# Performance work log

Measured on AMD Instinct MI355X. Metric: run time of the kernel, lower is better.

The kernel has to match this reference:

```python
import jax, jax.numpy as jnp
import numpy as np


def setup_inputs() -> dict:
    key = jax.random.key(0)
    ks = jax.random.split(key, 6)
    B, S, D = 2, 2048, 1024
    E, DFF = 8, 2048  # E includes always-on expert 0; router sees E-1 routed experts
    scale = 0.02
    return {
        "hidden_states": jax.random.normal(ks[0], (B, S, D), dtype=jnp.float32),
        "router_w": jax.random.normal(ks[1], (D, E - 1), dtype=jnp.float32) * scale,
        "router_b": jnp.zeros((E - 1,), dtype=jnp.float32),
        "wg": jax.random.normal(ks[2], (E, D, DFF), dtype=jnp.float32) * scale,
        "wu": jax.random.normal(ks[3], (E, D, DFF), dtype=jnp.float32) * scale,
        "wd": jax.random.normal(ks[4], (E, DFF, D), dtype=jnp.float32) * scale,
        "top_k": 2,
    }


def _expert_mlp(x, wg_e, wu_e, wd_e):
    # SwiGLU MLP: down( silu(x @ gate) * (x @ up) )
    return (jax.nn.silu(x @ wg_e) * (x @ wu_e)) @ wd_e


def reference(hidden_states, router_w, router_b, wg, wu, wd, top_k):
    B, S, D = hidden_states.shape
    E = wg.shape[0]  # total experts incl. always-on expert 0
    x = hidden_states.reshape(-1, D)  # [T, D]
    T = x.shape[0]

    # Router over E-1 routed experts, softmax in float32
    router_logits = x @ router_w + router_b  # [T, E-1]
    probs = jax.nn.softmax(router_logits.astype(jnp.float32), axis=-1)
    topw, topi = jax.lax.top_k(probs, top_k)  # [T, k]
    topw = topw / jnp.sum(topw, axis=-1, keepdims=True)
    topw = topw.astype(x.dtype)

    # Dense combine weights over routed experts (0 for unselected)
    cw = jnp.zeros((T, E - 1), dtype=x.dtype)
    cw = cw.at[jnp.arange(T)[:, None], topi].add(topw)  # [T, E-1]

    # Always-on expert 0 with weight 1
    out = _expert_mlp(x, wg[0], wu[0], wd[0])  # [T, D]

    # Routed experts 1..E-1 (static small loop over experts)
    for e in range(1, E):
        ye = _expert_mlp(x, wg[e], wu[e], wd[e])  # [T, D]
        out = out + cw[:, e - 1, None] * ye

    return out.reshape(B, S, -1)
```

## Files before the change

kernel.cpp:

```cpp
#include <hip/hip_runtime.h>

#define T_TOK 4096
#define DIM   1024
#define DFF   2048
#define NE    8
#define NR    7
#define MAXNB 71
#define NY    (32 + MAXNB)

typedef __bf16 bf16x8 __attribute__((ext_vector_type(8)));
typedef float  floatx4 __attribute__((ext_vector_type(4)));

__device__ __forceinline__ unsigned short f32_bf16(float f) {
  union { float f; unsigned int u; } v; v.f = f;
  unsigned int u = v.u;
  unsigned int r = (u + 0x7FFFu + ((u >> 16) & 1u)) >> 16;
  return (unsigned short)r;
}

typedef __attribute__((address_space(3))) void lds_void_t;
typedef const __attribute__((address_space(1))) void g_void_t;

__device__ __forceinline__ void gld16(const void* g, void* l) {
  __builtin_amdgcn_global_load_lds((g_void_t*)g, (lds_void_t*)l, 16, 0, 0);
}

__global__ __launch_bounds__(256) void cvt_x_kernel(const float4* __restrict__ in,
                                                    ushort4* __restrict__ out) {
  int i = blockIdx.x * 256 + threadIdx.x;
  float4 v = in[i];
  ushort4 o;
  o.x = f32_bf16(v.x); o.y = f32_bf16(v.y);
  o.z = f32_bf16(v.z); o.w = f32_bf16(v.w);
  out[i] = o;
}

__global__ __launch_bounds__(256) void router_kernel(const float* __restrict__ x,
                                                     const float* __restrict__ rw,
                                                     const float* __restrict__ rb,
                                                     int* __restrict__ idxAll,
                                                     float* __restrict__ wslAll,
                                                     int* __restrict__ cnt) {
  const int lane = threadIdx.x & 63;
  const int t = blockIdx.x * 4 + (threadIdx.x >> 6);
  const float* xr = x + (size_t)t * DIM;
  float acc[NR];
#pragma unroll
  for (int e = 0; e < NR; e++) acc[e] = 0.f;
  for (int d = lane; d < DIM; d += 64) {
    float xv = xr[d];
#pragma unroll
    for (int e = 0; e < NR; e++) acc[e] += xv * rw[d * NR + e];
  }
#pragma unroll
  for (int off = 32; off > 0; off >>= 1) {
#pragma unroll
    for (int e = 0; e < NR; e++) acc[e] += __shfl_xor(acc[e], off, 64);
  }
  if (lane == 0) {
    idxAll[t] = t; wslAll[t] = 1.0f;
    float lg[NR];
    float m = -1e30f;
#pragma unroll
    for (int e = 0; e < NR; e++) { lg[e] = acc[e] + rb[e]; m = fmaxf(m, lg[e]); }
    float p[NR], s = 0.f;
#pragma unroll
    for (int e = 0; e < NR; e++) { p[e] = expf(lg[e] - m); s += p[e]; }
#pragma unroll
    for (int e = 0; e < NR; e++) p[e] /= s;
    int i1 = 0;
#pragma unroll
    for (int e = 1; e < NR; e++) if (p[e] > p[i1]) i1 = e;
    int i2 = (i1 == 0) ? 1 : 0;
#pragma unroll
    for (int e = 0; e < NR; e++) if (e != i1 && p[e] > p[i2]) i2 = e;
    float w1 = p[i1], w2 = p[i2], sw = w1 + w2;
    int s1 = atomicAdd(&cnt[i1], 1);
    idxAll[4096 + i1 * 4096 + s1] = t; wslAll[4096 + i1 * 4096 + s1] = w1 / sw;
    int s2 = atomicAdd(&cnt[i2], 1);
    idxAll[4096 + i2 * 4096 + s2] = t; wslAll[4096 + i2 * 4096 + s2] = w2 / sw;
  }
}

__global__ __launch_bounds__(256) void sched_kernel(const int* __restrict__ cnt,
                                                    int* __restrict__ idxAll,
                                                    float* __restrict__ wslAll,
                                                    int4* __restrict__ schedAll,
                                                    int4* __restrict__ schedP,
                                                    int rsb) {
  __shared__ int nb[NR], pref[NR];
  if (threadIdx.x == 0) {
    int p = 0;
    for (int e = 0; e < NR; e++) { int c = cnt[e]; int n = (c + 127) >> 7; nb[e] = n; pref[e] = p; p += n; }
  }
  __syncthreads();
  for (int e = 0; e < NR; e++) {
    int c = cnt[e], top = nb[e] * 128;
    for (int i = c + (int)threadIdx.x; i < top; i += 256) {
      idxAll[4096 + e * 4096 + i] = 0; wslAll[4096 + e * 4096 + i] = 0.f;
    }
  }
  const int NBtot = pref[NR - 1] + nb[NR - 1];
  for (int y = threadIdx.x; y < 32; y += 256) {
    int4 ent; ent.x = 0; ent.y = y * 128; ent.z = y * 128; ent.w = 0;
    schedAll[y] = ent;
  }
  for (int y = threadIdx.x; y < MAXNB; y += 256) {
    int4 ent; ent.x = -1; ent.y = 0; ent.z = 0; ent.w = 0;
    if (y < NBtot) {
#pragma unroll
      for (int e = 0; e < NR; e++)
        if (y >= pref[e] && y < pref[e] + nb[e]) {
          int rb2 = y - pref[e];
          ent.x = e + 1; ent.y = 4096 + e * 4096 + rb2 * 128; ent.z = rsb + y * 128;
        }
    }
    schedAll[32 + y] = ent;
  }
  for (int i = threadIdx.x; i < NR * 32; i += 256) {
    int e = i >> 5, rb2 = i & 31;
    int4 ent; ent.w = 0;
    if (rb2 < nb[e]) { ent.x = e + 1; ent.y = 4096 + e * 4096 + rb2 * 128; ent.z = rsb + rb2 * 128; }
    else             { ent.x = -1; ent.y = 0; ent.z = 0; }
    schedP[i] = ent;
  }
}

__global__ __launch_bounds__(256) void transpose_cvt_kernel(
    const float* __restrict__ wg, const float* __restrict__ wu, const float* __restrict__ wd,
    unsigned short* __restrict__ wgt, unsigned short* __restrict__ wut,
    unsigned short* __restrict__ wdt) {
  __shared__ float tile[64][33];
  const int z = blockIdx.z;
  const float* src; unsigned short* dst; int R, C;
  if (z < 8)       { src = wg + (size_t)z * DIM * DFF;        dst = wgt + (size_t)z * DIM * DFF;        R = DIM; C = DFF; }
  else if (z < 16) { src = wu + (size_t)(z - 8) * DIM * DFF;  dst = wut + (size_t)(z - 8) * DIM * DFF;  R = DIM; C = DFF; }
  else             { src = wd + (size_t)(z - 16) * DFF * DIM; dst = wdt + (size_t)(z - 16) * DFF * DIM; R = DFF; C = DIM; }
  const int c0 = blockIdx.x * 32, r0 = blockIdx.y * 64;
  if (c0 >= C || r0 >= R) return;
  const int tx = threadIdx.x & 31, ty = threadIdx.x >> 5;
#pragma unroll
  for (int j = ty; j < 64; j += 8)
    tile[j][tx] = src[(size_t)(r0 + j) * C + c0 + tx];
  __syncthreads();
#pragma unroll
  for (int j = ty; j < 32; j += 8) {
    unsigned int lo = f32_bf16(tile[2 * tx][j]);
    unsigned int hi = f32_bf16(tile[2 * tx + 1][j]);
    *(unsigned int*)(dst + (size_t)(c0 + j) * R + r0 + 2 * tx) = lo | (hi << 16);
  }
}

__global__ __launch_bounds__(256) void gemm1_kernel(
    const unsigned short* __restrict__ xb, const unsigned short* __restrict__ wgt,
    const unsigned short* __restrict__ wut, const int* __restrict__ idxAll,
    const int4* __restrict__ sched, unsigned short* __restrict__ h) {
  const int4 ent = sched[blockIdx.y];
  if (ent.x < 0) return;
  __shared__ unsigned short As[128 * 32];
  __shared__ unsigned short Bg[64 * 32];
  __shared__ unsigned short Bu[64 * 32];
  const int tid = threadIdx.x, lane = tid & 63, wid = tid >> 6;
  const int n0 = blockIdx.x * 64;
  const int wm = (wid >> 1) * 64, wn = (wid & 1) * 32;
  floatx4 accg[4][2], accu[4][2];
  const floatx4 z4 = {0.f, 0.f, 0.f, 0.f};
#pragma unroll
  for (int i = 0; i < 4; i++)
#pragma unroll
    for (int j = 0; j < 2; j++) { accg[i][j] = z4; accu[i][j] = z4; }
  const unsigned short* wgt_e = wgt + (size_t)ent.x * DIM * DFF;
  const unsigned short* wut_e = wut + (size_t)ent.x * DIM * DFF;
  const int srow = tid >> 2, scol = (tid & 3) * 8;
  const int tok0 = idxAll[ent.y + srow];
  const int tok1 = idxAll[ent.y + srow + 64];
  const unsigned short* ap0 = xb + (size_t)tok0 * DIM + scol;
  const unsigned short* ap1 = xb + (size_t)tok1 * DIM + scol;
  const unsigned short* bgp = wgt_e + (size_t)(n0 + srow) * DIM + scol;
  const unsigned short* bup = wut_e + (size_t)(n0 + srow) * DIM + scol;
  unsigned short* as0 = As + tid * 8;
  unsigned short* as1 = As + (256 + tid) * 8;
  unsigned short* bgl = Bg + tid * 8;
  unsigned short* bul = Bu + tid * 8;
  const int fr = lane & 15, kq = (lane >> 4) * 8;
  for (int k0 = 0; k0 < DIM; k0 += 32) {
    __syncthreads();
    gld16(ap0 + k0, as0); gld16(ap1 + k0, as1);
    gld16(bgp + k0, bgl); gld16(bup + k0, bul);
    __syncthreads();
    bf16x8 af[4], bgf[2], buf2[2];
#pragma unroll
    for (int mi = 0; mi < 4; mi++) af[mi] = *(const bf16x8*)(As + (wm + mi * 16 + fr) * 32 + kq);
#pragma unroll
    for (int ni = 0; ni < 2; ni++) {
      bgf[ni]  = *(const bf16x8*)(Bg + (wn + ni * 16 + fr) * 32 + kq);
      buf2[ni] = *(const bf16x8*)(Bu + (wn + ni * 16 + fr) * 32 + kq);
    }
#pragma unroll
    for (int mi = 0; mi < 4; mi++)
#pragma unroll
      for (int ni = 0; ni < 2; ni++) {
        accg[mi][ni] = __builtin_amdgcn_mfma_f32_16x16x32_bf16(af[mi], bgf[ni], accg[mi][ni], 0, 0, 0);
        accu[mi][ni] = __builtin_amdgcn_mfma_f32_16x16x32_bf16(af[mi], buf2[ni], accu[mi][ni], 0, 0, 0);
      }
  }
  const int rb0 = wm + (lane >> 4) * 4;
  const int cb0 = n0 + wn + fr;
#pragma unroll
  for (int mi = 0; mi < 4; mi++)
#pragma unroll
    for (int ni = 0; ni < 2; ni++)
#pragma unroll
      for (int r = 0; r < 4; r++) {
        int lrow = rb0 + mi * 16 + r;
        int col = cb0 + ni * 16;
        float g = accg[mi][ni][r], u = accu[mi][ni][r];
        float hv = (g / (1.f + __expf(-g))) * u;
        h[(size_t)(ent.z + lrow) * DFF + col] = f32_bf16(hv);
      }
}

__global__ __launch_bounds__(256) void gemm2_kernel(
    const unsigned short* __restrict__ h, const unsigned short* __restrict__ wdt,
    const int* __restrict__ idxAll, const float* __restrict__ wslAll,
    const int4* __restrict__ sched, float* __restrict__ out) {
  const int4 ent = sched[blockIdx.y];
  if (ent.x < 0) return;
  __shared__ unsigned short As[128 * 32];
  __shared__ unsigned short Bs[128 * 32];
  const int tid = threadIdx.x, lane = tid & 63, wid = tid >> 6;
  const int n0 = blockIdx.x * 128;
  const int wm = (wid >> 1) * 64, wn = (wid & 1) * 64;
  floatx4 acc[4][4];
  const floatx4 z4 = {0.f, 0.f, 0.f, 0.f};
#pragma unroll
  for (int i = 0; i < 4; i++)
#pragma unroll
    for (int j = 0; j < 4; j++) acc[i][j] = z4;
  const unsigned short* wdt_e = wdt + (size_t)ent.x * DFF * DIM;
  const int srow = tid >> 2, scol = (tid & 3) * 8;
  const unsigned short* ap0 = h + (size_t)(ent.z + srow) * DFF + scol;
  const unsigned short* ap1 = ap0 + (size_t)64 * DFF;
  const unsigned short* bp0 = wdt_e + (size_t)(n0 + srow) * DFF + scol;
  const unsigned short* bp1 = bp0 + (size_t)64 * DFF;
  unsigned short* as0 = As + tid * 8;
  unsigned short* as1 = As + (256 + tid) * 8;
  unsigned short* bs0 = Bs + tid * 8;
  unsigned short* bs1 = Bs + (256 + tid) * 8;
  const int fr = lane & 15, kq = (lane >> 4) * 8;
  for (int k0 = 0; k0 < DFF; k0 += 32) {
    __syncthreads();
    gld16(ap0 + k0, as0); gld16(ap1 + k0, as1);
    gld16(bp0 + k0, bs0); gld16(bp1 + k0, bs1);
    __syncthreads();
    bf16x8 af[4], bf[4];
#pragma unroll
    for (int mi = 0; mi < 4; mi++) af[mi] = *(const bf16x8*)(As + (wm + mi * 16 + fr) * 32 + kq);
#pragma unroll
    for (int ni = 0; ni < 4; ni++) bf[ni] = *(const bf16x8*)(Bs + (wn + ni * 16 + fr) * 32 + kq);
#pragma unroll
    for (int mi = 0; mi < 4; mi++)
#pragma unroll
      for (int ni = 0; ni < 4; ni++)
        acc[mi][ni] = __builtin_amdgcn_mfma_f32_16x16x32_bf16(af[mi], bf[ni], acc[mi][ni], 0, 0, 0);
  }
  const int rb0 = wm + (lane >> 4) * 4;
  const int cb0 = n0 + wn + fr;
#pragma unroll
  for (int mi = 0; mi < 4; mi++)
#pragma unroll
    for (int r = 0; r < 4; r++) {
      int lrow = rb0 + mi * 16 + r;
      int tok = idxAll[ent.y + lrow];
      float s = wslAll[ent.y + lrow];
      if (s != 0.f) {
#pragma unroll
        for (int ni = 0; ni < 4; ni++)
          atomicAdd(&out[(size_t)tok * DIM + cb0 + ni * 16], s * acc[mi][ni][r]);
      }
    }
}

extern "C" void kernel_launch(void* const* d_in, const int* in_sizes, int n_in,
                              void* d_out, int out_size, void* d_ws, size_t ws_size,
                              hipStream_t stream) {
  const float* x  = (const float*)d_in[0];
  const float* rw = (const float*)d_in[1];
  const float* rb = (const float*)d_in[2];
  const float* wg = (const float*)d_in[3];
  const float* wu = (const float*)d_in[4];
  const float* wd = (const float*)d_in[5];
  float* out = (float*)d_out;

  const bool modeA = ws_size >= (size_t)163321408;
  const bool modeB = !modeA && ws_size >= (size_t)146544192;
  const size_t H_ROWS = modeA ? 13184 : (modeB ? 9088 : 4096);
  const int rsb = modeA ? 4096 : 0;

  char* p = (char*)d_ws;
  unsigned short* xb  = (unsigned short*)p; p += (size_t)T_TOK * DIM * 2;
  unsigned short* h   = (unsigned short*)p; p += H_ROWS * DFF * 2;
  unsigned short* wgt = (unsigned short*)p; p += (size_t)NE * DIM * DFF * 2;
  unsigned short* wut = (unsigned short*)p; p += (size_t)NE * DIM * DFF * 2;
  unsigned short* wdt = (unsigned short*)p; p += (size_t)NE * DIM * DFF * 2;
  int*   idxAll = (int*)p;   p += (size_t)(4096 + NR * 4096) * 4;
  float* wslAll = (float*)p; p += (size_t)(4096 + NR * 4096) * 4;
  int*   cnt = (int*)p;      p += 64;
  int4*  schedAll = (int4*)p; p += 2048;
  int4*  schedP   = (int4*)p; p += 4096;

  cvt_x_kernel<<<dim3(T_TOK * DIM / 4 / 256), 256, 0, stream>>>((const float4*)x, (ushort4*)xb);
  hipMemsetAsync(cnt, 0, 64, stream);
  hipMemsetAsync(out, 0, (size_t)out_size * 4, stream);
  router_kernel<<<dim3(T_TOK / 4), 256, 0, stream>>>(x, rw, rb, idxAll, wslAll, cnt);
  sched_kernel<<<dim3(1), 256, 0, stream>>>(cnt, idxAll, wslAll, schedAll, schedP, rsb);
  transpose_cvt_kernel<<<dim3(64, 32, 24), 256, 0, stream>>>(wg, wu, wd, wgt, wut, wdt);

  if (modeA) {
    gemm1_kernel<<<dim3(DFF / 64, NY), 256, 0, stream>>>(xb, wgt, wut, idxAll, schedAll, h);
    gemm2_kernel<<<dim3(DIM / 128, NY), 256, 0, stream>>>(h, wdt, idxAll, wslAll, schedAll, out);
  } else if (modeB) {
    gemm1_kernel<<<dim3(DFF / 64, 32), 256, 0, stream>>>(xb, wgt, wut, idxAll, schedAll, h);
    gemm2_kernel<<<dim3(DIM / 128, 32), 256, 0, stream>>>(h, wdt, idxAll, wslAll, schedAll, out);
    gemm1_kernel<<<dim3(DFF / 64, MAXNB), 256, 0, stream>>>(xb, wgt, wut, idxAll, schedAll + 32, h);
    gemm2_kernel<<<dim3(DIM / 128, MAXNB), 256, 0, stream>>>(h, wdt, idxAll, wslAll, schedAll + 32, out);
  } else {
    gemm1_kernel<<<dim3(DFF / 64, 32), 256, 0, stream>>>(xb, wgt, wut, idxAll, schedAll, h);
    gemm2_kernel<<<dim3(DIM / 128, 32), 256, 0, stream>>>(h, wdt, idxAll, wslAll, schedAll, out);
    for (int e = 0; e < NR; e++) {
      gemm1_kernel<<<dim3(DFF / 64, 32), 256, 0, stream>>>(xb, wgt, wut, idxAll, schedP + e * 32, h);
      gemm2_kernel<<<dim3(DIM / 128, 32), 256, 0, stream>>>(h, wdt, idxAll, wslAll, schedP + e * 32, out);
    }
  }
}
```

Baseline: 627.2 us.

## Replace atomic scatter-add with dense expert outputs plus combine kernel; widen gemm1 tile

In the large-workspace mode, gemm2 now writes per-row expert outputs densely into a scratch buffer that aliases the gate-weight copy once gemm1 is done. A new combine kernel then gathers each token's shared-expert row and its two routed rows and applies the routing weights, which removes the float atomics and the output memset. gemm1 moves to a 128-column tile with launch bounds set for 2 blocks per CU, doubling the reuse of A loads. The shared expert's token indices are now computed directly instead of read from an index array. This adds an extra pass over a large fp32 buffer and more register pressure in gemm1, and it relies on careful buffer aliasing (routing weights placed in wdt, y in wgt).

```diff
diff --git a/kernel.cpp b/kernel.cpp
--- a/kernel.cpp
+++ b/kernel.cpp
@@ -38,9 +38,11 @@
 __global__ __launch_bounds__(256) void router_kernel(const float* __restrict__ x,
                                                      const float* __restrict__ rw,
                                                      const float* __restrict__ rb,
-                                                     int* __restrict__ idxAll,
-                                                     float* __restrict__ wslAll,
-                                                     int* __restrict__ cnt) {
+                                                     int* __restrict__ idxR,
+                                                     float* __restrict__ wslR,
+                                                     int* __restrict__ cnt,
+                                                     int4* __restrict__ tokE,
+                                                     float2* __restrict__ tokW) {
   const int lane = threadIdx.x & 63;
   const int t = blockIdx.x * 4 + (threadIdx.x >> 6);
   const float* xr = x + (size_t)t * DIM;
@@ -58,7 +60,6 @@
     for (int e = 0; e < NR; e++) acc[e] += __shfl_xor(acc[e], off, 64);
   }
   if (lane == 0) {
-    idxAll[t] = t; wslAll[t] = 1.0f;
     float lg[NR];
     float m = -1e30f;
 #pragma unroll
@@ -75,18 +76,24 @@
 #pragma unroll
     for (int e = 0; e < NR; e++) if (e != i1 && p[e] > p[i2]) i2 = e;
     float w1 = p[i1], w2 = p[i2], sw = w1 + w2;
+    float w1n = w1 / sw, w2n = w2 / sw;
     int s1 = atomicAdd(&cnt[i1], 1);
-    idxAll[4096 + i1 * 4096 + s1] = t; wslAll[4096 + i1 * 4096 + s1] = w1 / sw;
+    idxR[i1 * 4096 + s1] = t; wslR[i1 * 4096 + s1] = w1n;
     int s2 = atomicAdd(&cnt[i2], 1);
-    idxAll[4096 + i2 * 4096 + s2] = t; wslAll[4096 + i2 * 4096 + s2] = w2 / sw;
+    idxR[i2 * 4096 + s2] = t; wslR[i2 * 4096 + s2] = w2n;
+    int4 te; te.x = i1; te.y = s1; te.z = i2; te.w = s2;
+    tokE[t] = te;
+    float2 tw; tw.x = w1n; tw.y = w2n;
+    tokW[t] = tw;
   }
 }
 
 __global__ __launch_bounds__(256) void sched_kernel(const int* __restrict__ cnt,
-                                                    int* __restrict__ idxAll,
-                                                    float* __restrict__ wslAll,
+                                                    int* __restrict__ idxR,
+                                                    float* __restrict__ wslR,
                                                     int4* __restrict__ schedAll,
                                                     int4* __restrict__ schedP,
+                                                    int* __restrict__ prefOut,
                                                     int rsb) {
   __shared__ int nb[NR], pref[NR];
   if (threadIdx.x == 0) {
@@ -94,15 +101,16 @@
     for (int e = 0; e < NR; e++) { int c = cnt[e]; int n = (c + 127) >> 7; nb[e] = n; pref[e] = p; p += n; }
   }
   __syncthreads();
+  if (threadIdx.x < NR) prefOut[threadIdx.x] = pref[threadIdx.x];
   for (int e = 0; e < NR; e++) {
     int c = cnt[e], top = nb[e] * 128;
     for (int i = c + (int)threadIdx.x; i < top; i += 256) {
-      idxAll[4096 + e * 4096 + i] = 0; wslAll[4096 + e * 4096 + i] = 0.f;
+      idxR[e * 4096 + i] = 0; wslR[e * 4096 + i] = 0.f;
     }
   }
   const int NBtot = pref[NR - 1] + nb[NR - 1];
   for (int y = threadIdx.x; y < 32; y += 256) {
-    int4 ent; ent.x = 0; ent.y = y * 128; ent.z = y * 128; ent.w = 0;
+    int4 ent; ent.x = 0; ent.y = -1; ent.z = y * 128; ent.w = 0;
     schedAll[y] = ent;
   }
   for (int y = threadIdx.x; y < MAXNB; y += 256) {
@@ -112,7 +120,7 @@
       for (int e = 0; e < NR; e++)
         if (y >= pref[e] && y < pref[e] + nb[e]) {
           int rb2 = y - pref[e];
-          ent.x = e + 1; ent.y = 4096 + e * 4096 + rb2 * 128; ent.z = rsb + y * 128;
+          ent.x = e + 1; ent.y = e * 4096 + rb2 * 128; ent.z = rsb + y * 128;
         }
     }
     schedAll[32 + y] = ent;
@@ -120,7 +128,7 @@
   for (int i = threadIdx.x; i < NR * 32; i += 256) {
     int e = i >> 5, rb2 = i & 31;
     int4 ent; ent.w = 0;
-    if (rb2 < nb[e]) { ent.x = e + 1; ent.y = 4096 + e * 4096 + rb2 * 128; ent.z = rsb + rb2 * 128; }
+    if (rb2 < nb[e]) { ent.x = e + 1; ent.y = e * 4096 + rb2 * 128; ent.z = rb2 * 128; }
     else             { ent.x = -1; ent.y = 0; ent.z = 0; }
     schedP[i] = ent;
   }
@@ -151,55 +159,61 @@
   }
 }
 
-__global__ __launch_bounds__(256) void gemm1_kernel(
+__global__ __launch_bounds__(256, 2) void gemm1_kernel(
     const unsigned short* __restrict__ xb, const unsigned short* __restrict__ wgt,
-    const unsigned short* __restrict__ wut, const int* __restrict__ idxAll,
+    const unsigned short* __restrict__ wut, const int* __restrict__ idxR,
     const int4* __restrict__ sched, unsigned short* __restrict__ h) {
   const int4 ent = sched[blockIdx.y];
   if (ent.x < 0) return;
   __shared__ unsigned short As[128 * 32];
-  __shared__ unsigned short Bg[64 * 32];
-  __shared__ unsigned short Bu[64 * 32];
+  __shared__ unsigned short Bg[128 * 32];
+  __shared__ unsigned short Bu[128 * 32];
   const int tid = threadIdx.x, lane = tid & 63, wid = tid >> 6;
-  const int n0 = blockIdx.x * 64;
-  const int wm = (wid >> 1) * 64, wn = (wid & 1) * 32;
-  floatx4 accg[4][2], accu[4][2];
+  const int n0 = blockIdx.x * 128;
+  const int wm = (wid >> 1) * 64, wn = (wid & 1) * 64;
+  floatx4 accg[4][4], accu[4][4];
   const floatx4 z4 = {0.f, 0.f, 0.f, 0.f};
 #pragma unroll
   for (int i = 0; i < 4; i++)
 #pragma unroll
-    for (int j = 0; j < 2; j++) { accg[i][j] = z4; accu[i][j] = z4; }
+    for (int j = 0; j < 4; j++) { accg[i][j] = z4; accu[i][j] = z4; }
   const unsigned short* wgt_e = wgt + (size_t)ent.x * DIM * DFF;
   const unsigned short* wut_e = wut + (size_t)ent.x * DIM * DFF;
   const int srow = tid >> 2, scol = (tid & 3) * 8;
-  const int tok0 = idxAll[ent.y + srow];
-  const int tok1 = idxAll[ent.y + srow + 64];
+  int tok0, tok1;
+  if (ent.y < 0) { tok0 = ent.z + srow; tok1 = ent.z + srow + 64; }
+  else           { tok0 = idxR[ent.y + srow]; tok1 = idxR[ent.y + srow + 64]; }
   const unsigned short* ap0 = xb + (size_t)tok0 * DIM + scol;
   const unsigned short* ap1 = xb + (size_t)tok1 * DIM + scol;
-  const unsigned short* bgp = wgt_e + (size_t)(n0 + srow) * DIM + scol;
-  const unsigned short* bup = wut_e + (size_t)(n0 + srow) * DIM + scol;
+  const unsigned short* bg0 = wgt_e + (size_t)(n0 + srow) * DIM + scol;
+  const unsigned short* bg1 = bg0 + (size_t)64 * DIM;
+  const unsigned short* bu0 = wut_e + (size_t)(n0 + srow) * DIM + scol;
+  const unsigned short* bu1 = bu0 + (size_t)64 * DIM;
   unsigned short* as0 = As + tid * 8;
   unsigned short* as1 = As + (256 + tid) * 8;
-  unsigned short* bgl = Bg + tid * 8;
-  unsigned short* bul = Bu + tid * 8;
+  unsigned short* bgl0 = Bg + tid * 8;
+  unsigned short* bgl1 = Bg + (256 + tid) * 8;
+  unsigned short* bul0 = Bu + tid * 8;
+  unsigned short* bul1 = Bu + (256 + tid) * 8;
   const int fr = lane & 15, kq = (lane >> 4) * 8;
   for (int k0 = 0; k0 < DIM; k0 += 32) {
     __syncthreads();
     gld16(ap0 + k0, as0); gld16(ap1 + k0, as1);
-    gld16(bgp + k0, bgl); gld16(bup + k0, bul);
-    __syncthreads();
-    bf16x8 af[4], bgf[2], buf2[2];
+    gld16(bg0 + k0, bgl0); gld16(bg1 + k0, bgl1);
+    gld16(bu0 + k0, bul0); gld16(bu1 + k0, bul1);
+    __syncthreads();
+    bf16x8 af[4], bgf[4], buf2[4];
 #pragma unroll
     for (int mi = 0; mi < 4; mi++) af[mi] = *(const bf16x8*)(As + (wm + mi * 16 + fr) * 32 + kq);
 #pragma unroll
-    for (int ni = 0; ni < 2; ni++) {
+    for (int ni = 0; ni < 4; ni++) {
       bgf[ni]  = *(const bf16x8*)(Bg + (wn + ni * 16 + fr) * 32 + kq);
       buf2[ni] = *(const bf16x8*)(Bu + (wn + ni * 16 + fr) * 32 + kq);
     }
 #pragma unroll
     for (int mi = 0; mi < 4; mi++)
 #pragma unroll
-      for (int ni = 0; ni < 2; ni++) {
+      for (int ni = 0; ni < 4; ni++) {
         accg[mi][ni] = __builtin_amdgcn_mfma_f32_16x16x32_bf16(af[mi], bgf[ni], accg[mi][ni], 0, 0, 0);
         accu[mi][ni] = __builtin_amdgcn_mfma_f32_16x16x32_bf16(af[mi], buf2[ni], accu[mi][ni], 0, 0, 0);
       }
@@ -209,7 +223,7 @@
 #pragma unroll
   for (int mi = 0; mi < 4; mi++)
 #pragma unroll
-    for (int ni = 0; ni < 2; ni++)
+    for (int ni = 0; ni < 4; ni++)
 #pragma unroll
       for (int r = 0; r < 4; r++) {
         int lrow = rb0 + mi * 16 + r;
@@ -222,8 +236,7 @@
 
 __global__ __launch_bounds__(256) void gemm2_kernel(
     const unsigned short* __restrict__ h, const unsigned short* __restrict__ wdt,
-    const int* __restrict__ idxAll, const float* __restrict__ wslAll,
-    const int4* __restrict__ sched, float* __restrict__ out) {
+    const int4* __restrict__ sched, float* __restrict__ y) {
   const int4 ent = sched[blockIdx.y];
   if (ent.x < 0) return;
   __shared__ unsigned short As[128 * 32];
@@ -269,16 +282,102 @@
 #pragma unroll
   for (int mi = 0; mi < 4; mi++)
 #pragma unroll
+    for (int ni = 0; ni < 4; ni++)
+#pragma unroll
+      for (int r = 0; r < 4; r++) {
+        int lrow = rb0 + mi * 16 + r;
+        y[(size_t)(ent.z + lrow) * DIM + cb0 + ni * 16] = acc[mi][ni][r];
+      }
+}
+
+__global__ __launch_bounds__(256) void gemm2_atomic_kernel(
+    const unsigned short* __restrict__ h, const unsigned short* __restrict__ wdt,
+    const int* __restrict__ idxR, const float* __restrict__ wslR,
+    const int4* __restrict__ sched, float* __restrict__ out) {
+  const int4 ent = sched[blockIdx.y];
+  if (ent.x < 0) return;
+  __shared__ unsigned short As[128 * 32];
+  __shared__ unsigned short Bs[128 * 32];
+  const int tid = threadIdx.x, lane = tid & 63, wid = tid >> 6;
+  const int n0 = blockIdx.x * 128;
+  const int wm = (wid >> 1) * 64, wn = (wid & 1) * 64;
+  floatx4 acc[4][4];
+  const floatx4 z4 = {0.f, 0.f, 0.f, 0.f};
+#pragma unroll
+  for (int i = 0; i < 4; i++)
+#pragma unroll
+    for (int j = 0; j < 4; j++) acc[i][j] = z4;
+  const unsigned short* wdt_e = wdt + (size_t)ent.x * DFF * DIM;
+  const int srow = tid >> 2, scol = (tid & 3) * 8;
+  const unsigned short* ap0 = h + (size_t)(ent.z + srow) * DFF + scol;
+  const unsigned short* ap1 = ap0 + (size_t)64 * DFF;
+  const unsigned short* bp0 = wdt_e + (size_t)(n0 + srow) * DFF + scol;
+  const unsigned short* bp1 = bp0 + (size_t)64 * DFF;
+  unsigned short* as0 = As + tid * 8;
+  unsigned short* as1 = As + (256 + tid) * 8;
+  unsigned short* bs0 = Bs + tid * 8;
+  unsigned short* bs1 = Bs + (256 + tid) * 8;
+  const int fr = lane & 15, kq = (lane >> 4) * 8;
+  for (int k0 = 0; k0 < DFF; k0 += 32) {
+    __syncthreads();
+    gld16(ap0 + k0, as0); gld16(ap1 + k0, as1);
+    gld16(bp0 + k0, bs0); gld16(bp1 + k0, bs1);
+    __syncthreads();
+    bf16x8 af[4], bf[4];
+#pragma unroll
+    for (int mi = 0; mi < 4; mi++) af[mi] = *(const bf16x8*)(As + (wm + mi * 16 + fr) * 32 + kq);
+#pragma unroll
+    for (int ni = 0; ni < 4; ni++) bf[ni] = *(const bf16x8*)(Bs + (wn + ni * 16 + fr) * 32 + kq);
+#pragma unroll
+    for (int mi = 0; mi < 4; mi++)
+#pragma unroll
+      for (int ni = 0; ni < 4; ni++)
+        acc[mi][ni] = __builtin_amdgcn_mfma_f32_16x16x32_bf16(af[mi], bf[ni], acc[mi][ni], 0, 0, 0);
+  }
+  const int rb0 = wm + (lane >> 4) * 4;
+  const int cb0 = n0 + wn + fr;
+#pragma unroll
+  for (int mi = 0; mi < 4; mi++)
+#pragma unroll
     for (int r = 0; r < 4; r++) {
       int lrow = rb0 + mi * 16 + r;
-      int tok = idxAll[ent.y + lrow];
-      float s = wslAll[ent.y + lrow];
-      if (s != 0.f) {
+      if (ent.y < 0) {
+        int tok = ent.z + lrow;
 #pragma unroll
         for (int ni = 0; ni < 4; ni++)
-          atomicAdd(&out[(size_t)tok * DIM + cb0 + ni * 16], s * acc[mi][ni][r]);
+          out[(size_t)tok * DIM + cb0 + ni * 16] = acc[mi][ni][r];
+      } else {
+        int tok = idxR[ent.y + lrow];
+        float s = wslR[ent.y + lrow];
+        if (s != 0.f) {
+#pragma unroll
+          for (int ni = 0; ni < 4; ni++)
+            atomicAdd(&out[(size_t)tok * DIM + cb0 + ni * 16], s * acc[mi][ni][r]);
+        }
       }
     }
+}
+
+__global__ __launch_bounds__(256) void combine_kernel(const float* __restrict__ y,
+                                                      const int4* __restrict__ tokE,
+                                                      const float2* __restrict__ tokW,
+                                                      const int* __restrict__ pref,
+                                                      float* __restrict__ out) {
+  const int t = blockIdx.x;
+  const int c = threadIdx.x * 4;
+  int4 te = tokE[t];
+  float2 tw = tokW[t];
+  int p1 = 4096 + pref[te.x] * 128 + te.y;
+  int p2 = 4096 + pref[te.z] * 128 + te.w;
+  float4 a = *(const float4*)(y + (size_t)t * DIM + c);
+  float4 b = *(const float4*)(y + (size_t)p1 * DIM + c);
+  float4 d = *(const float4*)(y + (size_t)p2 * DIM + c);
+  float4 o;
+  o.x = a.x + tw.x * b.x + tw.y * d.x;
+  o.y = a.y + tw.x * b.y + tw.y * d.y;
+  o.z = a.z + tw.x * b.z + tw.y * d.z;
+  o.w = a.w + tw.x * b.w + tw.y * d.w;
+  *(float4*)(out + (size_t)t * DIM + c) = o;
 }
 
 extern "C" void kernel_launch(void* const* d_in, const int* in_sizes, int n_in,
@@ -292,44 +391,50 @@
   const float* wd = (const float*)d_in[5];
   float* out = (float*)d_out;
 
-  const bool modeA = ws_size >= (size_t)163321408;
-  const bool modeB = !modeA && ws_size >= (size_t)146544192;
+  const bool modeA = ws_size >= (size_t)163300000;
+  const bool modeB = !modeA && ws_size >= (size_t)146700000;
   const size_t H_ROWS = modeA ? 13184 : (modeB ? 9088 : 4096);
   const int rsb = modeA ? 4096 : 0;
 
   char* p = (char*)d_ws;
   unsigned short* xb  = (unsigned short*)p; p += (size_t)T_TOK * DIM * 2;
   unsigned short* h   = (unsigned short*)p; p += H_ROWS * DFF * 2;
-  unsigned short* wgt = (unsigned short*)p; p += (size_t)NE * DIM * DFF * 2;
+  unsigned short* wgt = (unsigned short*)p;
+  float*          y   = (float*)p;          p += (size_t)NE * DIM * DFF * 2;
   unsigned short* wut = (unsigned short*)p; p += (size_t)NE * DIM * DFF * 2;
   unsigned short* wdt = (unsigned short*)p; p += (size_t)NE * DIM * DFF * 2;
-  int*   idxAll = (int*)p;   p += (size_t)(4096 + NR * 4096) * 4;
-  float* wslAll = (float*)p; p += (size_t)(4096 + NR * 4096) * 4;
-  int*   cnt = (int*)p;      p += 64;
+  int*   idxR = (int*)p;   p += (size_t)NR * 4096 * 4;
+  float* wslR;
+  if (modeA) { wslR = (float*)wdt; }
+  else       { wslR = (float*)p; p += (size_t)NR * 4096 * 4; }
+  int*   cnt  = (int*)p;      p += 64;
+  int*   pref = (int*)p;      p += 64;
   int4*  schedAll = (int4*)p; p += 2048;
   int4*  schedP   = (int4*)p; p += 4096;
+  int4*  tokE = (int4*)p;     p += (size_t)T_TOK * 16;
+  float2* tokW = (float2*)p;  p += (size_t)T_TOK * 8;
 
   cvt_x_kernel<<<dim3(T_TOK * DIM / 4 / 256), 256, 0, stream>>>((const float4*)x, (ushort4*)xb);
   hipMemsetAsync(cnt, 0, 64, stream);
-  hipMemsetAsync(out, 0, (size_t)out_size * 4, stream);
-  router_kernel<<<dim3(T_TOK / 4), 256, 0, stream>>>(x, rw, rb, idxAll, wslAll, cnt);
-  sched_kernel<<<dim3(1), 256, 0, stream>>>(cnt, idxAll, wslAll, schedAll, schedP, rsb);
+  router_kernel<<<dim3(T_TOK / 4), 256, 0, stream>>>(x, rw, rb, idxR, wslR, cnt, tokE, tokW);
+  sched_kernel<<<dim3(1), 256, 0, stream>>>(cnt, idxR, wslR, schedAll, schedP, pref, rsb);
   transpose_cvt_kernel<<<dim3(64, 32, 24), 256, 0, stream>>>(wg, wu, wd, wgt, wut, wdt);
 
   if (modeA) {
-    gemm1_kernel<<<dim3(DFF / 64, NY), 256, 0, stream>>>(xb, wgt, wut, idxAll, schedAll, h);
-    gemm2_kernel<<<dim3(DIM / 128, NY), 256, 0, stream>>>(h, wdt, idxAll, wslAll, schedAll, out);
+    gemm1_kernel<<<dim3(DFF / 128, NY), 256, 0, stream>>>(xb, wgt, wut, idxR, schedAll, h);
+    gemm2_kernel<<<dim3(DIM / 128, NY), 256, 0, stream>>>(h, wdt, schedAll, y);
+    combine_kernel<<<dim3(T_TOK), 256, 0, stream>>>(y, tokE, tokW, pref, out);
   } else if (modeB) {
-    gemm1_kernel<<<dim3(DFF / 64, 32), 256, 0, stream>>>(xb, wgt, wut, idxAll, schedAll, h);
-    gemm2_kernel<<<dim3(DIM / 128, 32), 256, 0, stream>>>(h, wdt, idxAll, wslAll, schedAll, out);
-    gemm1_kernel<<<dim3(DFF / 64, MAXNB), 256, 0, stream>>>(xb, wgt, wut, idxAll, schedAll + 32, h);
-    gemm2_kernel<<<dim3(DIM / 128, MAXNB), 256, 0, stream>>>(h, wdt, idxAll, wslAll, schedAll + 32, out);
+    gemm1_kernel<<<dim3(DFF / 128, 32), 256, 0, stream>>>(xb, wgt, wut, idxR, schedAll, h);
+    gemm2_atomic_kernel<<<dim3(DIM / 128, 32), 256, 0, stream>>>(h, wdt, idxR, wslR, schedAll, out);
+    gemm1_kernel<<<dim3(DFF / 128, MAXNB), 256, 0, stream>>>(xb, wgt, wut, idxR, schedAll + 32, h);
+    gemm2_atomic_kernel<<<dim3(DIM / 128, MAXNB), 256, 0, stream>>>(h, wdt, idxR, wslR, schedAll + 32, out);
   } else {
-    gemm1_kernel<<<dim3(DFF / 64, 32), 256, 0, stream>>>(xb, wgt, wut, idxAll, schedAll, h);
-    gemm2_kernel<<<dim3(DIM / 128, 32), 256, 0, stream>>>(h, wdt, idxAll, wslAll, schedAll, out);
+    gemm1_kernel<<<dim3(DFF / 128, 32), 256, 0, stream>>>(xb, wgt, wut, idxR, schedAll, h);
+    gemm2_atomic_kernel<<<dim3(DIM / 128, 32), 256, 0, stream>>>(h, wdt, idxR, wslR, schedAll, out);
     for (int e = 0; e < NR; e++) {
-      gemm1_kernel<<<dim3(DFF / 64, 32), 256, 0, stream>>>(xb, wgt, wut, idxAll, schedP + e * 32, h);
-      gemm2_kernel<<<dim3(DIM / 128, 32), 256, 0, stream>>>(h, wdt, idxAll, wslAll, schedP + e * 32, out);
+      gemm1_kernel<<<dim3(DFF / 128, 32), 256, 0, stream>>>(xb, wgt, wut, idxR, schedP + e * 32, h);
+      gemm2_atomic_kernel<<<dim3(DIM / 128, 32), 256, 0, stream>>>(h, wdt, idxR, wslR, schedP + e * 32, out);
     }
   }
 }
```

Result: faster. 596.5 us (-4.9%).
